# Performance work log

Measured on AMD Instinct MI355X. Metric: run time of the kernel, lower is better.

Reference implementation:

```python
import jax, jax.numpy as jnp
import numpy as np

VOCAB, EMB, H, D3, CTX = 30522, 768, 1024, 128, 512

def setup_inputs() -> dict:
    key = jax.random.key(0)
    ks = jax.random.split(key, 12)
    B, S = 8, 64
    inp = {
        'decoder_input_ids': jax.random.randint(ks[0], (B, S), 0, VOCAB, dtype=jnp.int64) if jax.config.jax_enable_x64 else jax.random.randint(ks[0], (B, S), 0, VOCAB, dtype=jnp.int32),
        'decoder_attn_mask': jnp.ones((B, S), dtype=jnp.int32),
        'decoder_seq_type_id': jnp.zeros((B, S), dtype=jnp.int32),
        'h_first': jax.random.normal(ks[1], (B, H), dtype=jnp.float32),
        'context': jax.random.normal(ks[2], (B, CTX, H), dtype=jnp.float32),
        # learned parameters (torch Linear stored transposed as [in, out])
        'emb_table': jax.random.normal(ks[3], (VOCAB, EMB), dtype=jnp.float32) * 0.02,
        'W_in': jax.random.normal(ks[4], (EMB, H), dtype=jnp.float32) * 0.02,
        'b_in': jnp.zeros((H,), dtype=jnp.float32),
        'W_s': jax.random.normal(ks[5], (H, H), dtype=jnp.float32) * 0.02,
        'b_s': jnp.zeros((H,), dtype=jnp.float32),
        'W_att_in': jax.random.normal(ks[6], (2 * H, D3), dtype=jnp.float32) * 0.02,
        'b_att_in': jnp.zeros((D3,), dtype=jnp.float32),
        'W_att_h': jax.random.normal(ks[7], (H, D3), dtype=jnp.float32) * 0.02,
        'b_att_h': jnp.zeros((D3,), dtype=jnp.float32),
        'V': jax.random.uniform(ks[8], (D3,), dtype=jnp.float32, minval=-1.0, maxval=1.0),
    }
    return inp


def reference(decoder_input_ids, decoder_attn_mask, decoder_seq_type_id, h_first,
              context, emb_table, W_in, b_in, W_s, b_s,
              W_att_in, b_att_in, W_att_h, b_att_h, V):
    # bert_embedding stub: plain token embedding lookup -> [B, S, 768]
    feats = emb_table[decoder_input_ids]
    # hidden_dense(context) is constant across steps; hoist it (same math)
    ctx_proj = context @ W_att_h + b_att_h          # [B, ctx, d3]
    h0 = context[:, -1, :]                          # initial recurrent state
    xs = jnp.swapaxes(feats, 0, 1)                  # [S, B, 768]

    def step(h, t_i):
        h = h @ W_s + b_s                           # dense_s
        s = jnp.concatenate([t_i @ W_in + b_in, h], axis=1)   # [B, 2H]
        a = jnp.tanh((s @ W_att_in + b_att_in)[:, None, :] + ctx_proj)  # [B,ctx,d3]
        att_before = jnp.einsum('d,bcd->bc', V, a)  # bmm(v, a^T) squeezed -> [B, ctx]
        # faithful to original: softmax over dim=1 of [B,1,ctx] (size-1 axis -> all ones)
        att_after = jax.nn.softmax(att_before[:, None, :], axis=1)[:, 0, :]
        idx = jnp.argmax(att_after, axis=1)         # ties -> 0, matches torch .max(1)
        return h, (att_before, idx)

    _, (atts, prts) = jax.lax.scan(step, h0, xs)
    atts = jnp.swapaxes(atts, 0, 1)                 # stack(dim=1).squeeze() -> [B, S, ctx]
    return atts, prts
```

## Files before the change

kernel.cpp:

```cpp
#include <hip/hip_runtime.h>
#include <hip/hip_bf16.h>

#define EMB 768
#define HD 1024
#define D3 128
#define CTXN 512
#define BB 8
#define SS 64

typedef __attribute__((ext_vector_type(8))) short short8v;
typedef __attribute__((ext_vector_type(4))) float f32x4;

__device__ __forceinline__ float fast_tanh(float x) {
  float e = __expf(2.f * x);
  return 1.f - 2.f * __builtin_amdgcn_rcpf(e + 1.f);
}
__device__ __forceinline__ float bf2f(__hip_bfloat16 x) { return __bfloat162float(x); }

struct GDesc {
  const void* A;
  const __hip_bfloat16* BT;
  const int* arowmap;
  const float* addrow_f;
  const float* bias_f;
  float* Cf;
  __hip_bfloat16* Cb;
  __hip_bfloat16* CbT;
  float* brow_f;
  int M, N, K, lda, ldbt, ldct, af32, mtiles, blk0, nblks;
};
struct GBatch { GDesc d[10]; int nd; };

__global__ __launch_bounds__(256) void gemmz(GBatch bat) {
  int bx = blockIdx.x;
  GDesc d = bat.d[0];
  for (int i = 1; i < bat.nd; ++i)
    if (bx >= bat.d[i].blk0) d = bat.d[i];
  int local = bx - d.blk0;
  int mt = local % d.mtiles, nt = local / d.mtiles;
  int bm0 = mt * 32, bn0 = nt * 64;

  __shared__ __hip_bfloat16 As[2][32][128];
  __shared__ __hip_bfloat16 Bs[2][64][128];
  int tid = threadIdx.x, lane = tid & 63, wid = tid >> 6;
  int l16 = lane & 15, g = lane >> 4;
  int wm = (wid & 1) * 16, wn = (wid >> 1) * 32;
  int arow = tid >> 3, aseg = tid & 7;
  int brow = tid >> 2, bseg = tid & 3;
  f32x4 acc[2] = {};

  int agr = bm0 + arow;
  int asrc = (agr < d.M) ? (d.arowmap ? d.arowmap[agr] : agr) : -1;
  const float* Af = (const float*)d.A;
  const __hip_bfloat16* Ab = (const __hip_bfloat16*)d.A;

  float fa[16];
  short8v ba0 = {}, ba1 = {}, bb0 = {}, bb1 = {}, bb2 = {}, bb3 = {};
  int nk = d.K >> 7;

  auto LD = [&](int k0) {
    if (d.af32) {
      if (asrc >= 0) {
        const float* s = Af + (long)asrc * d.lda + k0 + aseg * 16;
#pragma unroll
        for (int j = 0; j < 16; ++j) fa[j] = s[j];
      } else {
#pragma unroll
        for (int j = 0; j < 16; ++j) fa[j] = 0.f;
      }
    } else {
      if (asrc >= 0) {
        const __hip_bfloat16* s = Ab + (long)asrc * d.lda + k0 + aseg * 16;
        ba0 = *(const short8v*)s;
        ba1 = *(const short8v*)(s + 8);
      } else {
        short8v z = {};
        ba0 = z; ba1 = z;
      }
    }
    const __hip_bfloat16* bsrc = d.BT + (long)(bn0 + brow) * d.ldbt + k0 + bseg * 32;
    bb0 = *(const short8v*)bsrc;
    bb1 = *(const short8v*)(bsrc + 8);
    bb2 = *(const short8v*)(bsrc + 16);
    bb3 = *(const short8v*)(bsrc + 24);
  };
  auto ST = [&](int buf) {
    int rs = arow & 7;
    if (d.af32) {
      __hip_bfloat16 t8[16];
#pragma unroll
      for (int j = 0; j < 16; ++j) t8[j] = __float2bfloat16(fa[j]);
      *(short8v*)&As[buf][arow][((2 * aseg) ^ rs) * 8] = *(short8v*)t8;
      *(short8v*)&As[buf][arow][((2 * aseg + 1) ^ rs) * 8] = *(short8v*)(t8 + 8);
    } else {
      *(short8v*)&As[buf][arow][((2 * aseg) ^ rs) * 8] = ba0;
      *(short8v*)&As[buf][arow][((2 * aseg + 1) ^ rs) * 8] = ba1;
    }
    int rb = brow & 7;
    *(short8v*)&Bs[buf][brow][((4 * bseg) ^ rb) * 8] = bb0;
    *(short8v*)&Bs[buf][brow][((4 * bseg + 1) ^ rb) * 8] = bb1;
    *(short8v*)&Bs[buf][brow][((4 * bseg + 2) ^ rb) * 8] = bb2;
    *(short8v*)&Bs[buf][brow][((4 * bseg + 3) ^ rb) * 8] = bb3;
  };

  LD(0);
  ST(0);
  __syncthreads();
  for (int it = 0; it < nk; ++it) {
    int cur = it & 1;
    if (it + 1 < nk) LD((it + 1) << 7);
    int ar = wm + l16;
    int ars = ar & 7;
#pragma unroll
    for (int kf = 0; kf < 4; ++kf) {
      short8v a = *(const short8v*)&As[cur][ar][((kf * 4 + g) ^ ars) * 8];
#pragma unroll
      for (int j = 0; j < 2; ++j) {
        int br = wn + j * 16 + l16;
        short8v b = *(const short8v*)&Bs[cur][br][((kf * 4 + g) ^ (br & 7)) * 8];
        acc[j] = __builtin_amdgcn_mfma_f32_16x16x32_bf16(a, b, acc[j], 0, 0, 0);
      }
    }
    if (it + 1 < nk) ST(cur ^ 1);
    __syncthreads();
  }

  float* Cs = (float*)&Bs[0][0][0];
  bool doT = (d.CbT != nullptr);
#pragma unroll
  for (int j = 0; j < 2; ++j)
#pragma unroll
    for (int r = 0; r < 4; ++r) {
      int gl = wm + g * 4 + r, cl = wn + j * 16 + l16;
      int grow = bm0 + gl, gcol = bn0 + cl;
      float v = acc[j][r];
      if (d.bias_f) v += d.bias_f[gcol];
      if (d.addrow_f && grow == d.M - 1) v += d.addrow_f[gcol];
      if (grow < d.M) {
        if (d.Cf) d.Cf[(long)grow * d.N + gcol] = v;
        if (d.Cb) d.Cb[(long)grow * d.N + gcol] = __float2bfloat16(v);
        if (d.brow_f && grow == d.M - 1) d.brow_f[gcol] = v;
      }
      if (doT) Cs[cl * 33 + gl] = v;
    }
  if (doT) {
    __syncthreads();
    int ctrows = d.M < 1024 ? d.M : 1024;
    int n = tid >> 2, ms = (tid & 3) * 8;
    int gm0 = bm0 + ms;
    __hip_bfloat16 t8[8];
#pragma unroll
    for (int jj = 0; jj < 8; ++jj) t8[jj] = __float2bfloat16(Cs[n * 33 + ms + jj]);
    if (gm0 + 7 < ctrows) {
      *(short8v*)&d.CbT[(long)(bn0 + n) * d.ldct + gm0] = *(short8v*)t8;
    } else {
#pragma unroll
      for (int jj = 0; jj < 8; ++jj)
        if (gm0 + jj < ctrows) d.CbT[(long)(bn0 + n) * d.ldct + gm0 + jj] = t8[jj];
    }
  }
}

__global__ __launch_bounds__(256) void kcast(const float* __restrict__ W_s,
                                             const float* __restrict__ b_s,
                                             const float* __restrict__ context,
                                             const float* __restrict__ b_in,
                                             const float* __restrict__ W_att_in,
                                             const float* __restrict__ b_att_in,
                                             const float* __restrict__ W_att_h,
                                             const int* __restrict__ ids,
                                             __hip_bfloat16* __restrict__ Mb0,
                                             __hip_bfloat16* __restrict__ Mb0T,
                                             __hip_bfloat16* __restrict__ Y0T,
                                             __hip_bfloat16* __restrict__ WahT,
                                             __hip_bfloat16* __restrict__ WaiT,
                                             __hip_bfloat16* __restrict__ Gb,
                                             float* __restrict__ qb,
                                             int* __restrict__ rowmap) {
  int blk = blockIdx.x, tid = threadIdx.x;
  __shared__ __hip_bfloat16 tl[64][65];
  __shared__ float red[2][128];

  auto TP = [&](const float* src, int R, int C, __hip_bfloat16* dst, int tr, int tc) {
    int r0 = tr * 64, c0 = tc * 64;
    {
      int r = tid >> 2, cs = (tid & 3) * 16;
      const float* s = src + (long)(r0 + r) * C + c0 + cs;
#pragma unroll
      for (int j = 0; j < 16; ++j) tl[cs + j][r] = __float2bfloat16(s[j]);
    }
    __syncthreads();
    {
      int c = tid >> 2, rs = (tid & 3) * 16;
      __hip_bfloat16 o[16];
#pragma unroll
      for (int j = 0; j < 16; ++j) o[j] = tl[c][rs + j];
      *(short8v*)&dst[(long)(c0 + c) * R + r0 + rs] = *(short8v*)&o[0];
      *(short8v*)&dst[(long)(c0 + c) * R + r0 + rs + 8] = *(short8v*)&o[8];
    }
  };

  if (blk < 256) {
    long base = (long)blk * 4096;
    for (int i = tid; i < 4096; i += 256)
      Mb0[base + i] = __float2bfloat16(W_s[base + i]);
  } else if (blk == 256) {
    for (int i = tid; i < HD; i += 256)
      Mb0[(long)HD * HD + i] = __float2bfloat16(b_s[i]);
  } else if (blk < 513) {
    int t = blk - 257;
    TP(W_s, 1024, 1024, Mb0T, t >> 4, t & 15);
  } else if (blk < 545) {
    int t = blk - 513;
    TP(W_att_in + (long)1024 * D3, 1024, 128, Y0T, t >> 1, t & 1);
  } else if (blk < 577) {
    int t = blk - 545;
    TP(W_att_h, 1024, 128, WahT, t >> 1, t & 1);
  } else if (blk < 609) {
    int t = blk - 577;
    TP(W_att_in, 1024, 128, WaiT, t >> 1, t & 1);
  } else if (blk == 609) {
    for (int i = tid; i < BB * HD; i += 256) {
      int b = i >> 10, k = i & 1023;
      Gb[i] = __float2bfloat16(context[((long)b * CTXN + CTXN - 1) * HD + k]);
    }
  } else if (blk == 610) {
    int dd = tid & 127, h = tid >> 7;
    float acc = 0.f;
    for (int k = h * 512; k < h * 512 + 512; ++k)
      acc += b_in[k] * W_att_in[k * D3 + dd];
    red[h][dd] = acc;
    __syncthreads();
    if (h == 0) qb[dd] = red[0][dd] + red[1][dd] + b_att_in[dd];
  } else {
    for (int i = tid; i < 512; i += 256) {
      int t = i >> 3, b = i & 7;
      rowmap[i] = ids[b * SS + t];
    }
  }
}

__global__ __launch_bounds__(256) void katt(const float* __restrict__ qF,
                                            const float* __restrict__ qH,
                                            const float* __restrict__ ctxp,
                                            const float* __restrict__ V,
                                            float* __restrict__ out) {
  int blk = blockIdx.x;
  int b = blk >> 5, tt = (blk >> 4) & 1, ct = blk & 15;
  int t0 = tt * 32, c0 = ct * 32;
  int tid = threadIdx.x;
  __shared__ float lq[32][128];
  __shared__ float lc[32][132];
  __shared__ float lv[128];
  for (int i = tid; i < 32 * 128; i += 256) {
    int r = i >> 7, d = i & 127;
    int t = t0 + r;
    lq[r][d] = qF[((long)t * 8 + b) * 128 + d] +
               qH[(((long)(t & 7)) * 64 + (t >> 3) * 8 + b) * 128 + d];
    lc[r][d] = ctxp[((long)b * CTXN + c0 + r) * D3 + d];
  }
  if (tid < 128) lv[tid] = V[tid];
  __syncthreads();
  int cl = tid & 31, tg = tid >> 5;
  float r[4] = {0.f, 0.f, 0.f, 0.f};
  for (int d4 = 0; d4 < 32; ++d4) {
    float4 cv = *reinterpret_cast<const float4*>(&lc[cl][d4 * 4]);
    float4 vv = *reinterpret_cast<const float4*>(&lv[d4 * 4]);
#pragma unroll
    for (int u = 0; u < 4; ++u) {
      int t = tg + u * 8;
      float4 qv = *reinterpret_cast<const float4*>(&lq[t][d4 * 4]);
      r[u] = fmaf(vv.x, fast_tanh(qv.x + cv.x), r[u]);
      r[u] = fmaf(vv.y, fast_tanh(qv.y + cv.y), r[u]);
      r[u] = fmaf(vv.z, fast_tanh(qv.z + cv.z), r[u]);
      r[u] = fmaf(vv.w, fast_tanh(qv.w + cv.w), r[u]);
    }
  }
#pragma unroll
  for (int u = 0; u < 4; ++u) {
    int t = tg + u * 8;
    out[((long)b * SS + (t0 + t)) * CTXN + c0 + cl] = r[u];
  }
  if (blk == 0) {
    for (int i = tid; i < SS * BB; i += 256) out[(long)BB * SS * CTXN + i] = 0.f;
  }
}

static inline GDesc mk(const void* A, int af32, int lda, const int* arowmap,
                       const __hip_bfloat16* BT, int ldbt, int M, int N, int K,
                       const float* addrow_f, const float* bias_f, float* Cf,
                       __hip_bfloat16* Cb, __hip_bfloat16* CbT, int ldct,
                       float* brow_f, int blk0) {
  GDesc d;
  d.A = A; d.BT = BT; d.arowmap = arowmap;
  d.addrow_f = addrow_f; d.bias_f = bias_f;
  d.Cf = Cf; d.Cb = Cb; d.CbT = CbT; d.brow_f = brow_f;
  d.M = M; d.N = N; d.K = K; d.lda = lda; d.ldbt = ldbt; d.ldct = ldct;
  d.af32 = af32;
  d.mtiles = (M + 31) >> 5;
  d.blk0 = blk0;
  d.nblks = d.mtiles * (N >> 6);
  return d;
}

extern "C" void kernel_launch(void* const* d_in, const int* in_sizes, int n_in,
                              void* d_out, int out_size, void* d_ws, size_t ws_size,
                              hipStream_t stream) {
  const int* ids = (const int*)d_in[0];
  const float* context = (const float*)d_in[4];
  const float* emb = (const float*)d_in[5];
  const float* W_in = (const float*)d_in[6];
  const float* b_in = (const float*)d_in[7];
  const float* W_s = (const float*)d_in[8];
  const float* b_s = (const float*)d_in[9];
  const float* W_att_in = (const float*)d_in[10];
  const float* b_att_in = (const float*)d_in[11];
  const float* W_att_h = (const float*)d_in[12];
  const float* b_att_h = (const float*)d_in[13];
  const float* V = (const float*)d_in[14];

  float* ws = (float*)d_ws;
  float* ctxp = ws;
  float* Yf = ctxp + 524288;
  float* qF = Yf + 1180800;
  float* qH = qF + 65536;
  float* qb = qH + 65536;
  float* brow2 = qb + 128;
  float* brow4 = brow2 + 1024;
  float* brow8 = brow4 + 1024;
  float* brow16 = brow8 + 1024;
  float* brow32 = brow16 + 1024;
  int* rowmap = (int*)(brow32 + 1024);
  __hip_bfloat16* bfp = (__hip_bfloat16*)(rowmap + 512);
  __hip_bfloat16* Mb0 = bfp;
  __hip_bfloat16* Mb0T = Mb0 + 1049600;
  __hip_bfloat16* Mb1 = Mb0T + 1048576;
  __hip_bfloat16* Mb1T = Mb1 + 1049600;
  __hip_bfloat16* Mb2 = Mb1T + 1048576;
  __hip_bfloat16* Mb2T = Mb2 + 1049600;
  __hip_bfloat16* Mb3 = Mb2T + 1048576;
  __hip_bfloat16* Mb3T = Mb3 + 1049600;
  __hip_bfloat16* YT = Mb3T + 1048576;
  __hip_bfloat16* WahT = YT + 9 * 131072;
  __hip_bfloat16* WaiT = WahT + 131072;
  __hip_bfloat16* WcT = WaiT + 131072;
  __hip_bfloat16* Gb = WcT + 131072;
  float* out = (float*)d_out;

  auto Yfr = [&](int r) { return Yf + (long)r * 131200; };
  auto YTs = [&](int r) { return YT + (long)r * 131072; };

  kcast<<<dim3(612), dim3(256), 0, stream>>>(W_s, b_s, context, b_in, W_att_in,
                                             b_att_in, W_att_h, ids, Mb0, Mb0T,
                                             YTs(0), WahT, WaiT, Gb, qb, rowmap);
  {
    GBatch bt{}; int c = 0;
    bt.d[0] = mk(Mb0, 0, 1024, nullptr, Mb0T, 1024, 1025, 1024, 1024, b_s, nullptr, nullptr, Mb1, Mb1T, 1024, brow2, c); c += bt.d[0].nblks;
    bt.d[1] = mk(Mb0, 0, 1024, nullptr, YTs(0), 1024, 1025, 128, 1024, nullptr, nullptr, Yfr(1), nullptr, YTs(1), 1024, nullptr, c); c += bt.d[1].nblks;
    bt.d[2] = mk(context, 1, 1024, nullptr, WahT, 1024, 4096, 128, 1024, nullptr, b_att_h, ctxp, nullptr, nullptr, 0, nullptr, c); c += bt.d[2].nblks;
    bt.d[3] = mk(W_in, 1, 1024, nullptr, WaiT, 1024, 768, 128, 1024, nullptr, nullptr, nullptr, nullptr, WcT, 768, nullptr, c); c += bt.d[3].nblks;
    bt.nd = 4;
    gemmz<<<dim3(c), dim3(256), 0, stream>>>(bt);
  }
  {
    GBatch bt{}; int c = 0;
    bt.d[0] = mk(Mb1, 0, 1024, nullptr, Mb1T, 1024, 1025, 1024, 1024, brow2, nullptr, nullptr, Mb2, Mb2T, 1024, brow4, c); c += bt.d[0].nblks;
    bt.d[1] = mk(Mb1, 0, 1024, nullptr, YTs(0), 1024, 1025, 128, 1024, nullptr, nullptr, Yfr(2), nullptr, YTs(2), 1024, nullptr, c); c += bt.d[1].nblks;
    bt.d[2] = mk(Mb1, 0, 1024, nullptr, YTs(1), 1024, 1025, 128, 1024, Yfr(1) + 131072, nullptr, Yfr(3), nullptr, YTs(3), 1024, nullptr, c); c += bt.d[2].nblks;
    bt.nd = 3;
    gemmz<<<dim3(c), dim3(256), 0, stream>>>(bt);
  }
  {
    GBatch bt{}; int c = 0;
    bt.d[0] = mk(Mb2, 0, 1024, nullptr, Mb2T, 1024, 1025, 1024, 1024, brow4, nullptr, nullptr, Mb3, Mb3T, 1024, brow8, c); c += bt.d[0].nblks;
    for (int s = 0; s < 4; ++s) {
      bt.d[1 + s] = mk(Mb2, 0, 1024, nullptr, YTs(s), 1024, 1025, 128, 1024,
                       (s == 0) ? nullptr : (Yfr(s) + 131072), nullptr,
                       Yfr(4 + s), nullptr, YTs(4 + s), 1024, nullptr, c);
      c += bt.d[1 + s].nblks;
    }
    bt.nd = 5;
    gemmz<<<dim3(c), dim3(256), 0, stream>>>(bt);
  }
  {
    GBatch bt{}; int c = 0;
    bt.d[0] = mk(Mb3, 0, 1024, nullptr, Mb3T, 1024, 1025, 1024, 1024, brow8, nullptr, nullptr, Mb1, Mb1T, 1024, brow16, c); c += bt.d[0].nblks;
    bt.d[1] = mk(Mb3, 0, 1024, nullptr, YTs(0), 1024, 1025, 128, 1024, nullptr, nullptr, Yfr(8), nullptr, YTs(8), 1024, nullptr, c); c += bt.d[1].nblks;
    bt.d[2] = mk(Gb, 0, 1024, nullptr, Mb3T, 1024, 8, 1024, 1024, nullptr, brow8, nullptr, Gb + 8192, nullptr, 0, nullptr, c); c += bt.d[2].nblks;
    bt.nd = 3;
    gemmz<<<dim3(c), dim3(256), 0, stream>>>(bt);
  }
  {
    GBatch bt{}; int c = 0;
    bt.d[0] = mk(Mb1, 0, 1024, nullptr, Mb1T, 1024, 1025, 1024, 1024, brow16, nullptr, nullptr, Mb2, Mb2T, 1024, brow32, c); c += bt.d[0].nblks;
    bt.d[1] = mk(Gb, 0, 1024, nullptr, Mb1T, 1024, 16, 1024, 1024, nullptr, brow16, nullptr, Gb + 16384, nullptr, 0, nullptr, c); c += bt.d[1].nblks;
    bt.nd = 2;
    gemmz<<<dim3(c), dim3(256), 0, stream>>>(bt);
  }
  {
    GBatch bt{}; int c = 0;
    bt.d[0] = mk(Gb, 0, 1024, nullptr, Mb2T, 1024, 32, 1024, 1024, nullptr, brow32, nullptr, Gb + 32768, nullptr, 0, nullptr, c); c += bt.d[0].nblks;
    bt.nd = 1;
    gemmz<<<dim3(c), dim3(256), 0, stream>>>(bt);
  }
  {
    GBatch bt{}; int c = 0;
    for (int r = 1; r <= 8; ++r) {
      bt.d[r - 1] = mk(Gb, 0, 1024, nullptr, YTs(r), 1024, 64, 128, 1024, nullptr,
                       Yfr(r) + 131072, qH + (long)(r - 1) * 8192, nullptr, nullptr,
                       0, nullptr, c);
      c += bt.d[r - 1].nblks;
    }
    bt.d[8] = mk(emb, 1, 768, rowmap, WcT, 768, 512, 128, 768, nullptr, qb, qF,
                 nullptr, nullptr, 0, nullptr, c);
    c += bt.d[8].nblks;
    bt.nd = 9;
    gemmz<<<dim3(c), dim3(256), 0, stream>>>(bt);
  }
  katt<<<dim3(256), dim3(256), 0, stream>>>(qF, qH, ctxp, V, out);
}
```

Measured before the change: 151.9 us.

## Replace M^32 power computation with repeated M^16 steps and move embedding GEMM earlier

```diff
diff --git a/kernel.cpp b/kernel.cpp
--- a/kernel.cpp
+++ b/kernel.cpp
@@ -329,8 +329,7 @@
   float* brow4 = brow2 + 1024;
   float* brow8 = brow4 + 1024;
   float* brow16 = brow8 + 1024;
-  float* brow32 = brow16 + 1024;
-  int* rowmap = (int*)(brow32 + 1024);
+  int* rowmap = (int*)(brow16 + 1024);
   __hip_bfloat16* bfp = (__hip_bfloat16*)(rowmap + 512);
   __hip_bfloat16* Mb0 = bfp;
   __hip_bfloat16* Mb0T = Mb0 + 1049600;
@@ -367,7 +366,8 @@
     bt.d[0] = mk(Mb1, 0, 1024, nullptr, Mb1T, 1024, 1025, 1024, 1024, brow2, nullptr, nullptr, Mb2, Mb2T, 1024, brow4, c); c += bt.d[0].nblks;
     bt.d[1] = mk(Mb1, 0, 1024, nullptr, YTs(0), 1024, 1025, 128, 1024, nullptr, nullptr, Yfr(2), nullptr, YTs(2), 1024, nullptr, c); c += bt.d[1].nblks;
     bt.d[2] = mk(Mb1, 0, 1024, nullptr, YTs(1), 1024, 1025, 128, 1024, Yfr(1) + 131072, nullptr, Yfr(3), nullptr, YTs(3), 1024, nullptr, c); c += bt.d[2].nblks;
-    bt.nd = 3;
+    bt.d[3] = mk(emb, 1, 768, rowmap, WcT, 768, 512, 128, 768, nullptr, qb, qF, nullptr, nullptr, 0, nullptr, c); c += bt.d[3].nblks;
+    bt.nd = 4;
     gemmz<<<dim3(c), dim3(256), 0, stream>>>(bt);
   }
   {
@@ -390,31 +390,32 @@
     bt.nd = 3;
     gemmz<<<dim3(c), dim3(256), 0, stream>>>(bt);
   }
+  for (int lev = 0; lev < 3; ++lev) {
+    GBatch bt{}; int c = 0;
+    bt.d[0] = mk(Gb + (long)lev * 16384, 0, 1024, nullptr, Mb1T, 1024, 16, 1024, 1024,
+                 nullptr, brow16, nullptr, Gb + (long)(lev + 1) * 16384, nullptr, 0,
+                 nullptr, c);
+    c += bt.d[0].nblks;
+    for (int r = 1; r <= 8; ++r) {
+      bt.d[r] = mk(Gb + (long)lev * 16384, 0, 1024, nullptr, YTs(r), 1024, 16, 128,
+                   1024, nullptr, Yfr(r) + 131072,
+                   qH + (long)(r - 1) * 8192 + (long)lev * 2048, nullptr, nullptr, 0,
+                   nullptr, c);
+      c += bt.d[r].nblks;
+    }
+    bt.nd = 9;
+    gemmz<<<dim3(c), dim3(256), 0, stream>>>(bt);
+  }
   {
     GBatch bt{}; int c = 0;
-    bt.d[0] = mk(Mb1, 0, 1024, nullptr, Mb1T, 1024, 1025, 1024, 1024, brow16, nullptr, nullptr, Mb2, Mb2T, 1024, brow32, c); c += bt.d[0].nblks;
-    bt.d[1] = mk(Gb, 0, 1024, nullptr, Mb1T, 1024, 16, 1024, 1024, nullptr, brow16, nullptr, Gb + 16384, nullptr, 0, nullptr, c); c += bt.d[1].nblks;
-    bt.nd = 2;
-    gemmz<<<dim3(c), dim3(256), 0, stream>>>(bt);
-  }
-  {
-    GBatch bt{}; int c = 0;
-    bt.d[0] = mk(Gb, 0, 1024, nullptr, Mb2T, 1024, 32, 1024, 1024, nullptr, brow32, nullptr, Gb + 32768, nullptr, 0, nullptr, c); c += bt.d[0].nblks;
-    bt.nd = 1;
-    gemmz<<<dim3(c), dim3(256), 0, stream>>>(bt);
-  }
-  {
-    GBatch bt{}; int c = 0;
     for (int r = 1; r <= 8; ++r) {
-      bt.d[r - 1] = mk(Gb, 0, 1024, nullptr, YTs(r), 1024, 64, 128, 1024, nullptr,
-                       Yfr(r) + 131072, qH + (long)(r - 1) * 8192, nullptr, nullptr,
-                       0, nullptr, c);
+      bt.d[r - 1] = mk(Gb + 49152, 0, 1024, nullptr, YTs(r), 1024, 16, 128, 1024,
+                       nullptr, Yfr(r) + 131072,
+                       qH + (long)(r - 1) * 8192 + 6144, nullptr, nullptr, 0,
+                       nullptr, c);
       c += bt.d[r - 1].nblks;
     }
-    bt.d[8] = mk(emb, 1, 768, rowmap, WcT, 768, 512, 128, 768, nullptr, qb, qF,
-                 nullptr, nullptr, 0, nullptr, c);
-    c += bt.d[8].nblks;
-    bt.nd = 9;
+    bt.nd = 8;
     gemmz<<<dim3(c), dim3(256), 0, stream>>>(bt);
   }
   katt<<<dim3(256), dim3(256), 0, stream>>>(qF, qH, ctxp, V, out);
```

New measurement: 162.1 us. 1.07x slower.

## Fold preprocessing cast kernel into GEMMs and restructure doubling-step schedule

Applied to the files above, without the earlier changes.

```diff
diff --git a/kernel.cpp b/kernel.cpp
--- a/kernel.cpp
+++ b/kernel.cpp
@@ -8,6 +8,7 @@
 #define BB 8
 #define SS 64
 
+typedef __hip_bfloat16 bf16;
 typedef __attribute__((ext_vector_type(8))) short short8v;
 typedef __attribute__((ext_vector_type(4))) float f32x4;
 
@@ -15,24 +16,26 @@
   float e = __expf(2.f * x);
   return 1.f - 2.f * __builtin_amdgcn_rcpf(e + 1.f);
 }
-__device__ __forceinline__ float bf2f(__hip_bfloat16 x) { return __bfloat162float(x); }
 
 struct GDesc {
   const void* A;
-  const __hip_bfloat16* BT;
-  const int* arowmap;
+  const float* alast;
+  const bf16* BT;
+  const float* Bf32;
+  const int* ids;
   const float* addrow_f;
   const float* bias_f;
-  float* Cf;
-  __hip_bfloat16* Cb;
-  __hip_bfloat16* CbT;
-  float* brow_f;
-  int M, N, K, lda, ldbt, ldct, af32, mtiles, blk0, nblks;
+  float* Cf; bf16* Cb; bf16* CbT; float* brow_f;
+  int M, N, K, lda, ldbt, ldct, af32, amode, bmode, mtiles, blk0, nblks;
 };
-struct GBatch { GDesc d[10]; int nd; };
+struct GBatch { GDesc d[12]; int nd; };
 
 __global__ __launch_bounds__(256) void gemmz(GBatch bat) {
-  int bx = blockIdx.x;
+  int nwg = gridDim.x, orig = blockIdx.x;
+  int q8 = nwg >> 3, r8 = nwg & 7;
+  int xcd = orig & 7, idx = orig >> 3;
+  int bx = (xcd < r8 ? xcd * (q8 + 1) : r8 * (q8 + 1) + (xcd - r8) * q8) + idx;
+
   GDesc d = bat.d[0];
   for (int i = 1; i < bat.nd; ++i)
     if (bx >= bat.d[i].blk0) d = bat.d[i];
@@ -40,54 +43,61 @@
   int mt = local % d.mtiles, nt = local / d.mtiles;
   int bm0 = mt * 32, bn0 = nt * 64;
 
-  __shared__ __hip_bfloat16 As[2][32][128];
-  __shared__ __hip_bfloat16 Bs[2][64][128];
+  __shared__ bf16 As[2][32][128];
+  __shared__ bf16 Bs[2][64][128];
   int tid = threadIdx.x, lane = tid & 63, wid = tid >> 6;
   int l16 = lane & 15, g = lane >> 4;
   int wm = (wid & 1) * 16, wn = (wid >> 1) * 32;
   int arow = tid >> 3, aseg = tid & 7;
   int brow = tid >> 2, bseg = tid & 3;
+  int kr = tid >> 1, nh = (tid & 1) * 32;
   f32x4 acc[2] = {};
 
   int agr = bm0 + arow;
-  int asrc = (agr < d.M) ? (d.arowmap ? d.arowmap[agr] : agr) : -1;
-  const float* Af = (const float*)d.A;
-  const __hip_bfloat16* Ab = (const __hip_bfloat16*)d.A;
-
-  float fa[16];
-  short8v ba0 = {}, ba1 = {}, bb0 = {}, bb1 = {}, bb2 = {}, bb3 = {};
+  const float* afp = nullptr;
+  const bf16* abf = nullptr;
+  if (agr < d.M) {
+    long asrc;
+    if (d.amode == 2) asrc = (long)agr * CTXN + (CTXN - 1);
+    else if (d.amode == 3) asrc = d.ids[(agr & 7) * SS + (agr >> 3)];
+    else asrc = agr;
+    if (d.alast && agr == d.M - 1) afp = d.alast;
+    else if (d.af32) afp = (const float*)d.A + asrc * d.lda;
+    else abf = (const bf16*)d.A + asrc * d.lda;
+  }
+
+  float fa[16] = {};
+  short8v ba0 = {}, ba1 = {};
+  short8v bb0 = {}, bb1 = {}, bb2 = {}, bb3 = {};
+  float fb[32];
   int nk = d.K >> 7;
 
   auto LD = [&](int k0) {
-    if (d.af32) {
-      if (asrc >= 0) {
-        const float* s = Af + (long)asrc * d.lda + k0 + aseg * 16;
-#pragma unroll
-        for (int j = 0; j < 16; ++j) fa[j] = s[j];
-      } else {
-#pragma unroll
-        for (int j = 0; j < 16; ++j) fa[j] = 0.f;
-      }
+    if (afp) {
+      const float* s = afp + k0 + aseg * 16;
+#pragma unroll
+      for (int j = 0; j < 16; ++j) fa[j] = s[j];
+    } else if (abf) {
+      const bf16* s = abf + k0 + aseg * 16;
+      ba0 = *(const short8v*)s;
+      ba1 = *(const short8v*)(s + 8);
+    }
+    if (d.bmode == 0) {
+      const bf16* bsrc = d.BT + (long)(bn0 + brow) * d.ldbt + k0 + bseg * 32;
+      bb0 = *(const short8v*)bsrc;
+      bb1 = *(const short8v*)(bsrc + 8);
+      bb2 = *(const short8v*)(bsrc + 16);
+      bb3 = *(const short8v*)(bsrc + 24);
     } else {
-      if (asrc >= 0) {
-        const __hip_bfloat16* s = Ab + (long)asrc * d.lda + k0 + aseg * 16;
-        ba0 = *(const short8v*)s;
-        ba1 = *(const short8v*)(s + 8);
-      } else {
-        short8v z = {};
-        ba0 = z; ba1 = z;
-      }
-    }
-    const __hip_bfloat16* bsrc = d.BT + (long)(bn0 + brow) * d.ldbt + k0 + bseg * 32;
-    bb0 = *(const short8v*)bsrc;
-    bb1 = *(const short8v*)(bsrc + 8);
-    bb2 = *(const short8v*)(bsrc + 16);
-    bb3 = *(const short8v*)(bsrc + 24);
+      const float* s = d.Bf32 + (long)(k0 + kr) * d.ldbt + bn0 + nh;
+#pragma unroll
+      for (int j = 0; j < 32; ++j) fb[j] = s[j];
+    }
   };
   auto ST = [&](int buf) {
     int rs = arow & 7;
     if (d.af32) {
-      __hip_bfloat16 t8[16];
+      bf16 t8[16];
 #pragma unroll
       for (int j = 0; j < 16; ++j) t8[j] = __float2bfloat16(fa[j]);
       *(short8v*)&As[buf][arow][((2 * aseg) ^ rs) * 8] = *(short8v*)t8;
@@ -96,11 +106,20 @@
       *(short8v*)&As[buf][arow][((2 * aseg) ^ rs) * 8] = ba0;
       *(short8v*)&As[buf][arow][((2 * aseg + 1) ^ rs) * 8] = ba1;
     }
-    int rb = brow & 7;
-    *(short8v*)&Bs[buf][brow][((4 * bseg) ^ rb) * 8] = bb0;
-    *(short8v*)&Bs[buf][brow][((4 * bseg + 1) ^ rb) * 8] = bb1;
-    *(short8v*)&Bs[buf][brow][((4 * bseg + 2) ^ rb) * 8] = bb2;
-    *(short8v*)&Bs[buf][brow][((4 * bseg + 3) ^ rb) * 8] = bb3;
+    if (d.bmode == 0) {
+      int rb = brow & 7;
+      *(short8v*)&Bs[buf][brow][((4 * bseg) ^ rb) * 8] = bb0;
+      *(short8v*)&Bs[buf][brow][((4 * bseg + 1) ^ rb) * 8] = bb1;
+      *(short8v*)&Bs[buf][brow][((4 * bseg + 2) ^ rb) * 8] = bb2;
+      *(short8v*)&Bs[buf][brow][((4 * bseg + 3) ^ rb) * 8] = bb3;
+    } else {
+      int c = kr >> 3, w = kr & 7;
+#pragma unroll
+      for (int j = 0; j < 32; ++j) {
+        int n = nh + j;
+        Bs[buf][n][((c ^ (n & 7)) << 3) | w] = __float2bfloat16(fb[j]);
+      }
+    }
   };
 
   LD(0);
@@ -148,7 +167,7 @@
     int ctrows = d.M < 1024 ? d.M : 1024;
     int n = tid >> 2, ms = (tid & 3) * 8;
     int gm0 = bm0 + ms;
-    __hip_bfloat16 t8[8];
+    bf16 t8[8];
 #pragma unroll
     for (int jj = 0; jj < 8; ++jj) t8[jj] = __float2bfloat16(Cs[n * 33 + ms + jj]);
     if (gm0 + 7 < ctrows) {
@@ -157,85 +176,6 @@
 #pragma unroll
       for (int jj = 0; jj < 8; ++jj)
         if (gm0 + jj < ctrows) d.CbT[(long)(bn0 + n) * d.ldct + gm0 + jj] = t8[jj];
-    }
-  }
-}
-
-__global__ __launch_bounds__(256) void kcast(const float* __restrict__ W_s,
-                                             const float* __restrict__ b_s,
-                                             const float* __restrict__ context,
-                                             const float* __restrict__ b_in,
-                                             const float* __restrict__ W_att_in,
-                                             const float* __restrict__ b_att_in,
-                                             const float* __restrict__ W_att_h,
-                                             const int* __restrict__ ids,
-                                             __hip_bfloat16* __restrict__ Mb0,
-                                             __hip_bfloat16* __restrict__ Mb0T,
-                                             __hip_bfloat16* __restrict__ Y0T,
-                                             __hip_bfloat16* __restrict__ WahT,
-                                             __hip_bfloat16* __restrict__ WaiT,
-                                             __hip_bfloat16* __restrict__ Gb,
-                                             float* __restrict__ qb,
-                                             int* __restrict__ rowmap) {
-  int blk = blockIdx.x, tid = threadIdx.x;
-  __shared__ __hip_bfloat16 tl[64][65];
-  __shared__ float red[2][128];
-
-  auto TP = [&](const float* src, int R, int C, __hip_bfloat16* dst, int tr, int tc) {
-    int r0 = tr * 64, c0 = tc * 64;
-    {
-      int r = tid >> 2, cs = (tid & 3) * 16;
-      const float* s = src + (long)(r0 + r) * C + c0 + cs;
-#pragma unroll
-      for (int j = 0; j < 16; ++j) tl[cs + j][r] = __float2bfloat16(s[j]);
-    }
-    __syncthreads();
-    {
-      int c = tid >> 2, rs = (tid & 3) * 16;
-      __hip_bfloat16 o[16];
-#pragma unroll
-      for (int j = 0; j < 16; ++j) o[j] = tl[c][rs + j];
-      *(short8v*)&dst[(long)(c0 + c) * R + r0 + rs] = *(short8v*)&o[0];
-      *(short8v*)&dst[(long)(c0 + c) * R + r0 + rs + 8] = *(short8v*)&o[8];
-    }
-  };
-
-  if (blk < 256) {
-    long base = (long)blk * 4096;
-    for (int i = tid; i < 4096; i += 256)
-      Mb0[base + i] = __float2bfloat16(W_s[base + i]);
-  } else if (blk == 256) {
-    for (int i = tid; i < HD; i += 256)
-      Mb0[(long)HD * HD + i] = __float2bfloat16(b_s[i]);
-  } else if (blk < 513) {
-    int t = blk - 257;
-    TP(W_s, 1024, 1024, Mb0T, t >> 4, t & 15);
-  } else if (blk < 545) {
-    int t = blk - 513;
-    TP(W_att_in + (long)1024 * D3, 1024, 128, Y0T, t >> 1, t & 1);
-  } else if (blk < 577) {
-    int t = blk - 545;
-    TP(W_att_h, 1024, 128, WahT, t >> 1, t & 1);
-  } else if (blk < 609) {
-    int t = blk - 577;
-    TP(W_att_in, 1024, 128, WaiT, t >> 1, t & 1);
-  } else if (blk == 609) {
-    for (int i = tid; i < BB * HD; i += 256) {
-      int b = i >> 10, k = i & 1023;
-      Gb[i] = __float2bfloat16(context[((long)b * CTXN + CTXN - 1) * HD + k]);
-    }
-  } else if (blk == 610) {
-    int dd = tid & 127, h = tid >> 7;
-    float acc = 0.f;
-    for (int k = h * 512; k < h * 512 + 512; ++k)
-      acc += b_in[k] * W_att_in[k * D3 + dd];
-    red[h][dd] = acc;
-    __syncthreads();
-    if (h == 0) qb[dd] = red[0][dd] + red[1][dd] + b_att_in[dd];
-  } else {
-    for (int i = tid; i < 512; i += 256) {
-      int t = i >> 3, b = i & 7;
-      rowmap[i] = ids[b * SS + t];
     }
   }
 }
@@ -262,7 +202,7 @@
   if (tid < 128) lv[tid] = V[tid];
   __syncthreads();
   int cl = tid & 31, tg = tid >> 5;
-  float r[4] = {0.f, 0.f, 0.f, 0.f};
+  float r4[4] = {0.f, 0.f, 0.f, 0.f};
   for (int d4 = 0; d4 < 32; ++d4) {
     float4 cv = *reinterpret_cast<const float4*>(&lc[cl][d4 * 4]);
     float4 vv = *reinterpret_cast<const float4*>(&lv[d4 * 4]);
@@ -270,33 +210,33 @@
     for (int u = 0; u < 4; ++u) {
       int t = tg + u * 8;
       float4 qv = *reinterpret_cast<const float4*>(&lq[t][d4 * 4]);
-      r[u] = fmaf(vv.x, fast_tanh(qv.x + cv.x), r[u]);
-      r[u] = fmaf(vv.y, fast_tanh(qv.y + cv.y), r[u]);
-      r[u] = fmaf(vv.z, fast_tanh(qv.z + cv.z), r[u]);
-      r[u] = fmaf(vv.w, fast_tanh(qv.w + cv.w), r[u]);
+      r4[u] = fmaf(vv.x, fast_tanh(qv.x + cv.x), r4[u]);
+      r4[u] = fmaf(vv.y, fast_tanh(qv.y + cv.y), r4[u]);
+      r4[u] = fmaf(vv.z, fast_tanh(qv.z + cv.z), r4[u]);
+      r4[u] = fmaf(vv.w, fast_tanh(qv.w + cv.w), r4[u]);
     }
   }
 #pragma unroll
   for (int u = 0; u < 4; ++u) {
     int t = tg + u * 8;
-    out[((long)b * SS + (t0 + t)) * CTXN + c0 + cl] = r[u];
+    out[((long)b * SS + (t0 + t)) * CTXN + c0 + cl] = r4[u];
   }
   if (blk == 0) {
     for (int i = tid; i < SS * BB; i += 256) out[(long)BB * SS * CTXN + i] = 0.f;
   }
 }
 
-static inline GDesc mk(const void* A, int af32, int lda, const int* arowmap,
-                       const __hip_bfloat16* BT, int ldbt, int M, int N, int K,
-                       const float* addrow_f, const float* bias_f, float* Cf,
-                       __hip_bfloat16* Cb, __hip_bfloat16* CbT, int ldct,
-                       float* brow_f, int blk0) {
+static inline GDesc mkD(const void* A, int af32, int amode, int lda,
+                        const float* alast, const int* ids, const bf16* BT,
+                        const float* Bf32, int ldbt, int M, int N, int K,
+                        const float* addrow_f, const float* bias_f, float* Cf,
+                        bf16* Cb, bf16* CbT, int ldct, float* brow_f, int blk0) {
   GDesc d;
-  d.A = A; d.BT = BT; d.arowmap = arowmap;
+  d.A = A; d.alast = alast; d.BT = BT; d.Bf32 = Bf32; d.ids = ids;
   d.addrow_f = addrow_f; d.bias_f = bias_f;
   d.Cf = Cf; d.Cb = Cb; d.CbT = CbT; d.brow_f = brow_f;
   d.M = M; d.N = N; d.K = K; d.lda = lda; d.ldbt = ldbt; d.ldct = ldct;
-  d.af32 = af32;
+  d.af32 = af32; d.amode = amode; d.bmode = Bf32 ? 1 : 0;
   d.mtiles = (M + 31) >> 5;
   d.blk0 = blk0;
   d.nblks = d.mtiles * (N >> 6);
@@ -318,103 +258,104 @@
   const float* W_att_h = (const float*)d_in[12];
   const float* b_att_h = (const float*)d_in[13];
   const float* V = (const float*)d_in[14];
+  const float* Wa_bot = W_att_in + (long)1024 * D3;
 
   float* ws = (float*)d_ws;
   float* ctxp = ws;
-  float* Yf = ctxp + 524288;
-  float* qF = Yf + 1180800;
-  float* qH = qF + 65536;
-  float* qb = qH + 65536;
-  float* brow2 = qb + 128;
-  float* brow4 = brow2 + 1024;
-  float* brow8 = brow4 + 1024;
-  float* brow16 = brow8 + 1024;
-  float* brow32 = brow16 + 1024;
-  int* rowmap = (int*)(brow32 + 1024);
-  __hip_bfloat16* bfp = (__hip_bfloat16*)(rowmap + 512);
-  __hip_bfloat16* Mb0 = bfp;
-  __hip_bfloat16* Mb0T = Mb0 + 1049600;
-  __hip_bfloat16* Mb1 = Mb0T + 1048576;
-  __hip_bfloat16* Mb1T = Mb1 + 1049600;
-  __hip_bfloat16* Mb2 = Mb1T + 1048576;
-  __hip_bfloat16* Mb2T = Mb2 + 1049600;
-  __hip_bfloat16* Mb3 = Mb2T + 1048576;
-  __hip_bfloat16* Mb3T = Mb3 + 1049600;
-  __hip_bfloat16* YT = Mb3T + 1048576;
-  __hip_bfloat16* WahT = YT + 9 * 131072;
-  __hip_bfloat16* WaiT = WahT + 131072;
-  __hip_bfloat16* WcT = WaiT + 131072;
-  __hip_bfloat16* Gb = WcT + 131072;
+  float* qF = ws + 524288;
+  float* qH = ws + 589824;
+  float* qb = ws + 655360;
+  float* brow2 = ws + 655488;
+  float* brow4 = ws + 656512;
+  float* brow8 = ws + 657536;
+  float* brow16 = ws + 658560;
+  float* brow32 = ws + 659584;
+  float* zb = ws + 660608;
+  bf16* bfp = (bf16*)(ws + 661760);
+  bf16* Mb1 = bfp;
+  bf16* Mb1T = Mb1 + 1049600;
+  bf16* Mb2 = Mb1T + 1048576;
+  bf16* Mb2T = Mb2 + 1049600;
+  bf16* Mb3 = Mb2T + 1048576;
+  bf16* Mb3T = Mb3 + 1049600;
+  bf16* YT = Mb3T + 1048576;
+  bf16* WcT = YT + 9 * 131072;
+  bf16* Gb = WcT + 98304;
   float* out = (float*)d_out;
 
-  auto Yfr = [&](int r) { return Yf + (long)r * 131200; };
   auto YTs = [&](int r) { return YT + (long)r * 131072; };
-
-  kcast<<<dim3(612), dim3(256), 0, stream>>>(W_s, b_s, context, b_in, W_att_in,
-                                             b_att_in, W_att_h, ids, Mb0, Mb0T,
-                                             YTs(0), WahT, WaiT, Gb, qb, rowmap);
-  {
-    GBatch bt{}; int c = 0;
-    bt.d[0] = mk(Mb0, 0, 1024, nullptr, Mb0T, 1024, 1025, 1024, 1024, b_s, nullptr, nullptr, Mb1, Mb1T, 1024, brow2, c); c += bt.d[0].nblks;
-    bt.d[1] = mk(Mb0, 0, 1024, nullptr, YTs(0), 1024, 1025, 128, 1024, nullptr, nullptr, Yfr(1), nullptr, YTs(1), 1024, nullptr, c); c += bt.d[1].nblks;
-    bt.d[2] = mk(context, 1, 1024, nullptr, WahT, 1024, 4096, 128, 1024, nullptr, b_att_h, ctxp, nullptr, nullptr, 0, nullptr, c); c += bt.d[2].nblks;
-    bt.d[3] = mk(W_in, 1, 1024, nullptr, WaiT, 1024, 768, 128, 1024, nullptr, nullptr, nullptr, nullptr, WcT, 768, nullptr, c); c += bt.d[3].nblks;
+  auto zbr = [&](int r) { return zb + (long)r * 128; };
+
+  {
+    GBatch bt{}; int c = 0;
+    bt.d[0] = mkD(W_s, 1, 0, 1024, b_s, nullptr, nullptr, W_s, 1024, 1025, 1024, 1024, b_s, nullptr, nullptr, Mb1, Mb1T, 1024, brow2, c); c += bt.d[0].nblks;
+    bt.d[1] = mkD(W_s, 1, 0, 1024, b_s, nullptr, nullptr, Wa_bot, 128, 1025, 128, 1024, nullptr, nullptr, nullptr, nullptr, YTs(1), 1024, zbr(1), c); c += bt.d[1].nblks;
+    bt.d[2] = mkD(context, 1, 0, 1024, nullptr, nullptr, nullptr, W_att_h, 128, 4096, 128, 1024, nullptr, b_att_h, ctxp, nullptr, nullptr, 0, nullptr, c); c += bt.d[2].nblks;
+    bt.d[3] = mkD(W_in, 1, 0, 1024, nullptr, nullptr, nullptr, W_att_in, 128, 768, 128, 1024, nullptr, nullptr, nullptr, nullptr, WcT, 768, nullptr, c); c += bt.d[3].nblks;
+    bt.d[4] = mkD(b_in, 1, 0, 1024, nullptr, nullptr, nullptr, W_att_in, 128, 1, 128, 1024, nullptr, b_att_in, qb, nullptr, nullptr, 0, nullptr, c); c += bt.d[4].nblks;
+    bt.nd = 5;
+    gemmz<<<dim3(c), dim3(256), 0, stream>>>(bt);
+  }
+  {
+    GBatch bt{}; int c = 0;
+    bt.d[0] = mkD(Mb1, 0, 0, 1024, nullptr, nullptr, Mb1T, nullptr, 1024, 1025, 1024, 1024, brow2, nullptr, nullptr, Mb2, Mb2T, 1024, brow4, c); c += bt.d[0].nblks;
+    bt.d[1] = mkD(Mb1, 0, 0, 1024, nullptr, nullptr, nullptr, Wa_bot, 128, 1025, 128, 1024, nullptr, nullptr, nullptr, nullptr, YTs(2), 1024, zbr(2), c); c += bt.d[1].nblks;
+    bt.d[2] = mkD(Mb1, 0, 0, 1024, nullptr, nullptr, YTs(1), nullptr, 1024, 1025, 128, 1024, zbr(1), nullptr, nullptr, nullptr, YTs(3), 1024, zbr(3), c); c += bt.d[2].nblks;
+    bt.d[3] = mkD(emb, 1, 3, 768, nullptr, ids, WcT, nullptr, 768, 512, 128, 768, nullptr, qb, qF, nullptr, nullptr, 0, nullptr, c); c += bt.d[3].nblks;
     bt.nd = 4;
     gemmz<<<dim3(c), dim3(256), 0, stream>>>(bt);
   }
   {
     GBatch bt{}; int c = 0;
-    bt.d[0] = mk(Mb1, 0, 1024, nullptr, Mb1T, 1024, 1025, 1024, 1024, brow2, nullptr, nullptr, Mb2, Mb2T, 1024, brow4, c); c += bt.d[0].nblks;
-    bt.d[1] = mk(Mb1, 0, 1024, nullptr, YTs(0), 1024, 1025, 128, 1024, nullptr, nullptr, Yfr(2), nullptr, YTs(2), 1024, nullptr, c); c += bt.d[1].nblks;
-    bt.d[2] = mk(Mb1, 0, 1024, nullptr, YTs(1), 1024, 1025, 128, 1024, Yfr(1) + 131072, nullptr, Yfr(3), nullptr, YTs(3), 1024, nullptr, c); c += bt.d[2].nblks;
+    bt.d[0] = mkD(Mb2, 0, 0, 1024, nullptr, nullptr, Mb2T, nullptr, 1024, 1025, 1024, 1024, brow4, nullptr, nullptr, Mb3, Mb3T, 1024, brow8, c); c += bt.d[0].nblks;
+    bt.d[1] = mkD(Mb2, 0, 0, 1024, nullptr, nullptr, nullptr, Wa_bot, 128, 1025, 128, 1024, nullptr, nullptr, nullptr, nullptr, YTs(4), 1024, zbr(4), c); c += bt.d[1].nblks;
+    for (int s = 1; s <= 3; ++s) {
+      bt.d[1 + s] = mkD(Mb2, 0, 0, 1024, nullptr, nullptr, YTs(s), nullptr, 1024, 1025, 128, 1024, zbr(s), nullptr, nullptr, nullptr, YTs(4 + s), 1024, zbr(4 + s), c);
+      c += bt.d[1 + s].nblks;
+    }
+    bt.nd = 5;
+    gemmz<<<dim3(c), dim3(256), 0, stream>>>(bt);
+  }
+  {
+    GBatch bt{}; int c = 0;
+    bt.d[0] = mkD(Mb3, 0, 0, 1024, nullptr, nullptr, Mb3T, nullptr, 1024, 1025, 1024, 1024, brow8, nullptr, nullptr, Mb1, Mb1T, 1024, brow16, c); c += bt.d[0].nblks;
+    bt.d[1] = mkD(Mb3, 0, 0, 1024, nullptr, nullptr, nullptr, Wa_bot, 128, 1025, 128, 1024, nullptr, nullptr, nullptr, nullptr, YTs(8), 1024, zbr(8), c); c += bt.d[1].nblks;
+    bt.d[2] = mkD(context, 1, 2, 1024, nullptr, nullptr, Mb3T, nullptr, 1024, 8, 1024, 1024, nullptr, brow8, nullptr, Gb + 8192, nullptr, 0, nullptr, c); c += bt.d[2].nblks;
     bt.nd = 3;
     gemmz<<<dim3(c), dim3(256), 0, stream>>>(bt);
   }
   {
     GBatch bt{}; int c = 0;
-    bt.d[0] = mk(Mb2, 0, 1024, nullptr, Mb2T, 1024, 1025, 1024, 1024, brow4, nullptr, nullptr, Mb3, Mb3T, 1024, brow8, c); c += bt.d[0].nblks;
-    for (int s = 0; s < 4; ++s) {
-      bt.d[1 + s] = mk(Mb2, 0, 1024, nullptr, YTs(s), 1024, 1025, 128, 1024,
-                       (s == 0) ? nullptr : (Yfr(s) + 131072), nullptr,
-                       Yfr(4 + s), nullptr, YTs(4 + s), 1024, nullptr, c);
-      c += bt.d[1 + s].nblks;
-    }
-    bt.nd = 5;
-    gemmz<<<dim3(c), dim3(256), 0, stream>>>(bt);
-  }
-  {
-    GBatch bt{}; int c = 0;
-    bt.d[0] = mk(Mb3, 0, 1024, nullptr, Mb3T, 1024, 1025, 1024, 1024, brow8, nullptr, nullptr, Mb1, Mb1T, 1024, brow16, c); c += bt.d[0].nblks;
-    bt.d[1] = mk(Mb3, 0, 1024, nullptr, YTs(0), 1024, 1025, 128, 1024, nullptr, nullptr, Yfr(8), nullptr, YTs(8), 1024, nullptr, c); c += bt.d[1].nblks;
-    bt.d[2] = mk(Gb, 0, 1024, nullptr, Mb3T, 1024, 8, 1024, 1024, nullptr, brow8, nullptr, Gb + 8192, nullptr, 0, nullptr, c); c += bt.d[2].nblks;
-    bt.nd = 3;
-    gemmz<<<dim3(c), dim3(256), 0, stream>>>(bt);
-  }
-  {
-    GBatch bt{}; int c = 0;
-    bt.d[0] = mk(Mb1, 0, 1024, nullptr, Mb1T, 1024, 1025, 1024, 1024, brow16, nullptr, nullptr, Mb2, Mb2T, 1024, brow32, c); c += bt.d[0].nblks;
-    bt.d[1] = mk(Gb, 0, 1024, nullptr, Mb1T, 1024, 16, 1024, 1024, nullptr, brow16, nullptr, Gb + 16384, nullptr, 0, nullptr, c); c += bt.d[1].nblks;
-    bt.nd = 2;
-    gemmz<<<dim3(c), dim3(256), 0, stream>>>(bt);
-  }
-  {
-    GBatch bt{}; int c = 0;
-    bt.d[0] = mk(Gb, 0, 1024, nullptr, Mb2T, 1024, 32, 1024, 1024, nullptr, brow32, nullptr, Gb + 32768, nullptr, 0, nullptr, c); c += bt.d[0].nblks;
-    bt.nd = 1;
-    gemmz<<<dim3(c), dim3(256), 0, stream>>>(bt);
-  }
-  {
-    GBatch bt{}; int c = 0;
+    bt.d[0] = mkD(Mb1, 0, 0, 1024, nullptr, nullptr, Mb1T, nullptr, 1024, 1025, 1024, 1024, brow16, nullptr, nullptr, Mb2, Mb2T, 1024, brow32, c); c += bt.d[0].nblks;
+    bt.d[1] = mkD(context, 1, 2, 1024, nullptr, nullptr, Mb1T, nullptr, 1024, 8, 1024, 1024, nullptr, brow16, nullptr, Gb + 16384, nullptr, 0, nullptr, c); c += bt.d[1].nblks;
+    bt.d[2] = mkD(Gb + 8192, 0, 0, 1024, nullptr, nullptr, Mb1T, nullptr, 1024, 8, 1024, 1024, nullptr, brow16, nullptr, Gb + 24576, nullptr, 0, nullptr, c); c += bt.d[2].nblks;
     for (int r = 1; r <= 8; ++r) {
-      bt.d[r - 1] = mk(Gb, 0, 1024, nullptr, YTs(r), 1024, 64, 128, 1024, nullptr,
-                       Yfr(r) + 131072, qH + (long)(r - 1) * 8192, nullptr, nullptr,
-                       0, nullptr, c);
+      bt.d[2 + r] = mkD(context, 1, 2, 1024, nullptr, nullptr, YTs(r), nullptr, 1024, 8, 128, 1024, nullptr, zbr(r), qH + (long)(r - 1) * 8192, nullptr, nullptr, 0, nullptr, c);
+      c += bt.d[2 + r].nblks;
+    }
+    bt.nd = 11;
+    gemmz<<<dim3(c), dim3(256), 0, stream>>>(bt);
+  }
+  {
+    GBatch bt{}; int c = 0;
+    bt.d[0] = mkD(context, 1, 2, 1024, nullptr, nullptr, Mb2T, nullptr, 1024, 8, 1024, 1024, nullptr, brow32, nullptr, Gb + 32768, nullptr, 0, nullptr, c); c += bt.d[0].nblks;
+    bt.d[1] = mkD(Gb + 8192, 0, 0, 1024, nullptr, nullptr, Mb2T, nullptr, 1024, 8, 1024, 1024, nullptr, brow32, nullptr, Gb + 40960, nullptr, 0, nullptr, c); c += bt.d[1].nblks;
+    bt.d[2] = mkD(Gb + 16384, 0, 0, 1024, nullptr, nullptr, Mb2T, nullptr, 1024, 8, 1024, 1024, nullptr, brow32, nullptr, Gb + 49152, nullptr, 0, nullptr, c); c += bt.d[2].nblks;
+    bt.d[3] = mkD(Gb + 24576, 0, 0, 1024, nullptr, nullptr, Mb2T, nullptr, 1024, 8, 1024, 1024, nullptr, brow32, nullptr, Gb + 57344, nullptr, 0, nullptr, c); c += bt.d[3].nblks;
+    for (int r = 1; r <= 8; ++r) {
+      bt.d[3 + r] = mkD(Gb + 8192, 0, 0, 1024, nullptr, nullptr, YTs(r), nullptr, 1024, 24, 128, 1024, nullptr, zbr(r), qH + (long)(r - 1) * 8192 + 1024, nullptr, nullptr, 0, nullptr, c);
+      c += bt.d[3 + r].nblks;
+    }
+    bt.nd = 12;
+    gemmz<<<dim3(c), dim3(256), 0, stream>>>(bt);
+  }
+  {
+    GBatch bt{}; int c = 0;
+    for (int r = 1; r <= 8; ++r) {
+      bt.d[r - 1] = mkD(Gb + 32768, 0, 0, 1024, nullptr, nullptr, YTs(r), nullptr, 1024, 32, 128, 1024, nullptr, zbr(r), qH + (long)(r - 1) * 8192 + 4096, nullptr, nullptr, 0, nullptr, c);
       c += bt.d[r - 1].nblks;
     }
-    bt.d[8] = mk(emb, 1, 768, rowmap, WcT, 768, 512, 128, 768, nullptr, qb, qF,
-                 nullptr, nullptr, 0, nullptr, c);
-    c += bt.d[8].nblks;
-    bt.nd = 9;
+    bt.nd = 8;
     gemmz<<<dim3(c), dim3(256), 0, stream>>>(bt);
   }
   katt<<<dim3(256), dim3(256), 0, stream>>>(qF, qH, ctxp, V, out);
```

Measured after the change: 210.4 us. 1.38x slower.
